# Kernel tuning notes

Measured on AMD Instinct MI355X. Metric: run time of the kernel, lower is better.

## Reference

```python
import jax, jax.numpy as jnp
import numpy as np
import math

N_HEAD = 16
H_DIM = 32            # per-half head dim
LAMBDA_INIT = 0.8 - 0.6 * math.exp(-0.3 * 1)  # depth = 1
EPS = 1e-6


def _rmsnorm(x, scale):
    xf = x.astype(jnp.float32)
    normed = xf * jax.lax.rsqrt(jnp.mean(xf * xf, axis=-1, keepdims=True) + EPS)
    return normed.astype(x.dtype) * scale


def setup_inputs() -> dict:
    key = jax.random.key(0)
    ks = jax.random.split(key, 8)
    B, T, D = 2, 2048, 1024
    return {
        "x": jax.random.normal(ks[0], (B, T, D), jnp.float32),
        "Wqkv": jax.random.normal(ks[1], (D, 3 * D), jnp.float32) * (1.0 / math.sqrt(D)),
        "Wproj": jax.random.normal(ks[2], (D, D), jnp.float32) * (1.0 / math.sqrt(D)),
        "lambda_q1": jax.random.normal(ks[3], (H_DIM,), jnp.float32) * 0.1,
        "lambda_k1": jax.random.normal(ks[4], (H_DIM,), jnp.float32) * 0.1,
        "lambda_q2": jax.random.normal(ks[5], (H_DIM,), jnp.float32) * 0.1,
        "lambda_k2": jax.random.normal(ks[6], (H_DIM,), jnp.float32) * 0.1,
        "rms_scale": jnp.ones((2 * H_DIM,), jnp.float32),
    }


def reference(x, Wqkv, Wproj, lambda_q1, lambda_k1, lambda_q2, lambda_k2, rms_scale):
    B, T, C = x.shape
    H, h = N_HEAD, H_DIM
    qkv = x @ Wqkv                          # [B,T,3C]
    q, k, v = jnp.split(qkv, 3, axis=-1)
    q = q.reshape(B, T, 2 * H, h).transpose(0, 2, 1, 3)   # [B,2H,T,h]
    k = k.reshape(B, T, 2 * H, h).transpose(0, 2, 1, 3)   # [B,2H,T,h]
    v = v.reshape(B, T, H, 2 * h).transpose(0, 2, 1, 3)   # [B,H,T,2h]
    q1, q2 = jnp.split(q, 2, axis=1)        # each [B,H,T,h]
    k1, k2 = jnp.split(k, 2, axis=1)
    scale = 1.0 / math.sqrt(h)

    def sdpa(qh, kh):
        scores = jnp.einsum('bhqd,bhkd->bhqk', qh, kh) * scale
        return jnp.einsum('bhqk,bhkd->bhqd', jax.nn.softmax(scores, axis=-1), v)

    attn1 = sdpa(q1, k1)                    # [B,H,T,2h]
    attn2 = sdpa(q2, k2)
    lam1 = jnp.exp(jnp.sum(lambda_q1 * lambda_k1))
    lam2 = jnp.exp(jnp.sum(lambda_q2 * lambda_k2))
    lam = lam1 - lam2 + LAMBDA_INIT
    out = attn1 - lam * attn2
    out = _rmsnorm(out, rms_scale) * (1.0 - LAMBDA_INIT)
    out = out.transpose(0, 2, 1, 3).reshape(B, T, C)
    return out @ Wproj
```

## Files before the change

kernel.cpp:

```cpp
#include <hip/hip_runtime.h>
#include <cstdint>
#include <cstddef>


typedef short bf16x8 __attribute__((ext_vector_type(8)));
typedef float f32x4  __attribute__((ext_vector_type(4)));
typedef float f32x16 __attribute__((ext_vector_type(16)));
typedef unsigned short u16;
typedef u16 u16x4v __attribute__((ext_vector_type(4)));
typedef unsigned int u32;
typedef u32 u32x2 __attribute__((ext_vector_type(2)));
typedef u32 u32x4 __attribute__((ext_vector_type(4)));

#define LAMBDA_INIT 0.35550906759096926f
#define ONE_MINUS_LAMBDA_INIT 0.6444909324090307f
#define SCORE_SCALE 0.17677669529663687f

__device__ __forceinline__ u16 f2bf(float f) {
  uint32_t u = __float_as_uint(f);
  u += 0x7fffu + ((u >> 16) & 1u);
  return (u16)(u >> 16);
}

__device__ __forceinline__ void gload_lds16(const void* g, void* lds) {
  __builtin_amdgcn_global_load_lds(
      (const __attribute__((address_space(1))) void*)g,
      (__attribute__((address_space(3))) void*)lds, 16, 0, 0);
}

__device__ __forceinline__ u32 cvtpk_bf16(float lo, float hi) {
  u32 r;
  asm("v_cvt_pk_bf16_f32 %0, %1, %2" : "=v"(r) : "v"(lo), "v"(hi));
  return r;
}

__device__ __forceinline__ float xchg32f(float v, int hi) {
  u32x2 r = __builtin_amdgcn_permlane32_swap(__float_as_uint(v), __float_as_uint(v), false, false);
  return __uint_as_float(hi ? r.x : r.y);
}

__device__ __forceinline__ float rmax16(const f32x16& v) {
  float m = v[0];
#pragma unroll
  for (int i = 1; i < 16; ++i) m = fmaxf(m, v[i]);
  return m;
}

__device__ __forceinline__ float rsum16(const f32x16& v) {
  float a = 0.f;
#pragma unroll
  for (int i = 0; i < 16; ++i) a += v[i];
  return a;
}

__global__ void conv_x_kernel(const float* __restrict__ in, u16* __restrict__ out, int n4) {
  int i = blockIdx.x * blockDim.x + threadIdx.x;
  if (i < n4) {
    float4 v = ((const float4*)in)[i];
    u16x4v o;
    o.x = f2bf(v.x); o.y = f2bf(v.y); o.z = f2bf(v.z); o.w = f2bf(v.w);
    ((u16x4v*)out)[i] = o;
  }
}

__global__ void conv_transpose_kernel(const float* __restrict__ W, u16* __restrict__ WT,
                                      int K, int N) {
  __shared__ u16 L[64][72];
  const int n0 = blockIdx.x * 64, k0 = blockIdx.y * 64;
#pragma unroll
  for (int i = 0; i < 16; ++i) {
    int lin = i * 256 + threadIdx.x;
    int rr = lin >> 6, cc = lin & 63;
    L[rr][cc] = f2bf(W[(size_t)(k0 + rr) * N + n0 + cc]);
  }
  __syncthreads();
#pragma unroll
  for (int i = 0; i < 16; ++i) {
    int lin = i * 256 + threadIdx.x;
    int rr = lin >> 6, cc = lin & 63;
    WT[(size_t)(n0 + rr) * K + k0 + cc] = L[cc][rr];
  }
}

template <typename OutT>
__global__ __launch_bounds__(256, 2) void gemm_bt(const u16* __restrict__ A,
                                                  const u16* __restrict__ Bt,
                                                  OutT* __restrict__ C,
                                                  int M, int N, int K) {
  __shared__ __align__(16) u16 As[2][128 * 32];
  __shared__ __align__(16) u16 Bs[2][128 * 32];
  const int wid = threadIdx.x >> 6, lane = threadIdx.x & 63;
  const int l15 = lane & 15, lhi = lane >> 4;
  const int wm = wid >> 1, wn = wid & 1;
  const int tm = blockIdx.x * 128, tn = blockIdx.y * 128;
  const int rr = lane >> 2, cb = (lane & 3) * 8;
  const int nkt = K >> 5;

  f32x4 acc[4][4];
#pragma unroll
  for (int m = 0; m < 4; ++m)
#pragma unroll
    for (int n = 0; n < 4; ++n) acc[m][n] = (f32x4){0.f, 0.f, 0.f, 0.f};

  auto stage = [&](int buf, int kt) {
#pragma unroll
    for (int i = 0; i < 2; ++i) {
      int lr = wid * 32 + i * 16;
      gload_lds16(A + (size_t)(tm + lr + rr) * K + kt * 32 + cb, &As[buf][lr * 32]);
      gload_lds16(Bt + (size_t)(tn + lr + rr) * K + kt * 32 + cb, &Bs[buf][lr * 32]);
    }
  };

  stage(0, 0);
  __syncthreads();
  int buf = 0;
  for (int kt = 0; kt < nkt; ++kt) {
    if (kt + 1 < nkt) stage(buf ^ 1, kt + 1);
    bf16x8 af[4], bfr[4];
#pragma unroll
    for (int m = 0; m < 4; ++m)
      af[m] = *(const bf16x8*)&As[buf][(wm * 64 + m * 16 + l15) * 32 + lhi * 8];
#pragma unroll
    for (int n = 0; n < 4; ++n)
      bfr[n] = *(const bf16x8*)&Bs[buf][(wn * 64 + n * 16 + l15) * 32 + lhi * 8];
#pragma unroll
    for (int m = 0; m < 4; ++m)
#pragma unroll
      for (int n = 0; n < 4; ++n)
        acc[m][n] = __builtin_amdgcn_mfma_f32_16x16x32_bf16(af[m], bfr[n], acc[m][n], 0, 0, 0);
    __syncthreads();
    buf ^= 1;
  }

#pragma unroll
  for (int m = 0; m < 4; ++m)
#pragma unroll
    for (int n = 0; n < 4; ++n)
#pragma unroll
      for (int r = 0; r < 4; ++r) {
        int row = tm + wm * 64 + m * 16 + lhi * 4 + r;
        int col = tn + wn * 64 + n * 16 + l15;
        float v = acc[m][n][r];
        if constexpr (sizeof(OutT) == 2)
          C[(size_t)row * N + col] = (OutT)f2bf(v);
        else
          C[(size_t)row * N + col] = v;
      }
}

#define KLD 32
#define VLD 72

__global__ __launch_bounds__(256, 2) void diff_attn_kernel(
    const u16* __restrict__ qkv,
    const float* __restrict__ lq1, const float* __restrict__ lk1,
    const float* __restrict__ lq2, const float* __restrict__ lk2,
    const float* __restrict__ rms_scale,
    u16* __restrict__ y) {
  __shared__ __align__(16) u16 K1s[2][64 * KLD];
  __shared__ __align__(16) u16 K2s[2][64 * KLD];
  __shared__ __align__(16) u16 VTs[2][64 * VLD];

  const int tid = threadIdx.x;
  const int wid = tid >> 6, lane = tid & 63;
  const int l31 = lane & 31, hi = lane >> 5;

  const int id = blockIdx.x;
  const int swz = (id & 7) * 64 + (id >> 3);
  const int qt = swz & 15;
  const int bh = swz >> 4;
  const int b = bh >> 4, head = bh & 15;
  const size_t row0 = (size_t)b * 2048;

  float d1 = 0.f, d2 = 0.f;
#pragma unroll
  for (int i = 0; i < 32; ++i) { d1 += lq1[i] * lk1[i]; d2 += lq2[i] * lk2[i]; }
  const float lam = expf(d1) - expf(d2) + LAMBDA_INIT;

  const int qrow = qt * 128 + wid * 32 + l31;
  const u16* qrp = qkv + (row0 + qrow) * 3072;
  bf16x8 q1f[2], q2f[2];
#pragma unroll
  for (int c = 0; c < 2; ++c) {
    q1f[c] = *(const bf16x8*)(qrp + head * 32 + c * 16 + hi * 8);
    q2f[c] = *(const bf16x8*)(qrp + 512 + head * 32 + c * 16 + hi * 8);
  }

  f32x16 o1[2], o2[2];
#pragma unroll
  for (int dt = 0; dt < 2; ++dt)
#pragma unroll
    for (int i = 0; i < 16; ++i) { o1[dt][i] = 0.f; o2[dt][i] = 0.f; }
  float m1 = -1e30f, m2 = -1e30f;
  float ls1 = 0.f, ls2 = 0.f;

  auto issueK = [&](int buf, int kt) {
    const size_t krow0 = row0 + (size_t)kt * 64;
    const int srow = wid * 16 + (lane >> 2);
    const int gcol = 8 * ((lane & 3) ^ ((lane >> 3) & 3));
    const u16* g = qkv + (krow0 + srow) * 3072 + 1024 + head * 32 + gcol;
    gload_lds16(g, &K1s[buf][wid * 512]);
    gload_lds16(g + 512, &K2s[buf][wid * 512]);
  };
  auto loadV = [&](int kt, bf16x8* nv) {
    const size_t krow0 = row0 + (size_t)kt * 64;
#pragma unroll
    for (int h2 = 0; h2 < 2; ++h2) {
      int vid = h2 * 256 + tid;
      int vrow = vid >> 3, d0 = (vid & 7) * 8;
      nv[h2] = *(const bf16x8*)(qkv + (krow0 + vrow) * 3072 + 2048 + head * 64 + d0);
    }
  };
  auto writeV = [&](int buf, const bf16x8* nv) {
#pragma unroll
    for (int h2 = 0; h2 < 2; ++h2) {
      int vid = h2 * 256 + tid;
      int vrow = vid >> 3, d0 = (vid & 7) * 8;
      int wrow = vrow ^ (d0 & 56);
#pragma unroll
      for (int e = 0; e < 8; ++e) VTs[buf][(d0 + e) * VLD + wrow] = (u16)nv[h2][e];
    }
  };

  auto process = [&](const bf16x8* qf, const u16* Ks, const bf16x8 (*vf)[2][2],
                     float& m, float& ls, f32x16* o) {
    f32x16 s[2];
#pragma unroll
    for (int t = 0; t < 2; ++t) {
#pragma unroll
      for (int i = 0; i < 16; ++i) s[t][i] = 0.f;
      const int row = t * 32 + l31;
      const int sg = 8 * ((row >> 1) & 3);
#pragma unroll
      for (int c = 0; c < 2; ++c) {
        bf16x8 kf = *(const bf16x8*)&Ks[row * KLD + ((c * 16 + hi * 8) ^ sg)];
        s[t] = __builtin_amdgcn_mfma_f32_32x32x16_bf16(kf, qf[c], s[t], 0, 0, 0);
      }
    }
    float pm = fmaxf(rmax16(s[0]), rmax16(s[1]));
    pm = fmaxf(pm, xchg32f(pm, hi));
    if (!__all(pm - m <= 8.0f)) {
      float mn = fmaxf(m, pm);
      float corr = __expf((m - mn) * SCORE_SCALE);
      m = mn;
      ls *= corr;
#pragma unroll
      for (int dt = 0; dt < 2; ++dt)
#pragma unroll
        for (int i = 0; i < 16; ++i) o[dt][i] *= corr;
    }
#pragma unroll
    for (int t = 0; t < 2; ++t)
#pragma unroll
      for (int i = 0; i < 16; ++i)
        s[t][i] = __expf((s[t][i] - m) * SCORE_SCALE);
    ls += rsum16(s[0]) + rsum16(s[1]);
#pragma unroll
    for (int t = 0; t < 2; ++t) {
      u32 W[4][2];
#pragma unroll
      for (int g = 0; g < 4; ++g)
#pragma unroll
        for (int u = 0; u < 2; ++u)
          W[g][u] = cvtpk_bf16(s[t][4 * g + 2 * u], s[t][4 * g + 2 * u + 1]);
#pragma unroll
      for (int kap = 0; kap < 2; ++kap) {
        u32x2 r0 = __builtin_amdgcn_permlane32_swap(W[2 * kap][0], W[2 * kap + 1][0], false, false);
        u32x2 r1 = __builtin_amdgcn_permlane32_swap(W[2 * kap][1], W[2 * kap + 1][1], false, false);
        u32x4 words = {r0.x, r1.x, r0.y, r1.y};
        bf16x8 pB = __builtin_bit_cast(bf16x8, words);
#pragma unroll
        for (int dt = 0; dt < 2; ++dt)
          o[dt] = __builtin_amdgcn_mfma_f32_32x32x16_bf16(vf[t][kap][dt], pB, o[dt], 0, 0, 0);
      }
    }
  };

  {
    bf16x8 v0[2];
    issueK(0, 0);
    loadV(0, v0);
    writeV(0, v0);
  }
  __syncthreads();

  int buf = 0;
  for (int kt = 0; kt < 32; ++kt) {
    bf16x8 nv[2];
    if (kt + 1 < 32) { issueK(buf ^ 1, kt + 1); loadV(kt + 1, nv); }

    bf16x8 vf[2][2][2];
#pragma unroll
    for (int t = 0; t < 2; ++t)
#pragma unroll
      for (int kap = 0; kap < 2; ++kap)
#pragma unroll
        for (int dt = 0; dt < 2; ++dt) {
          int d = dt * 32 + l31;
          int koff = (t * 32 + kap * 16 + hi * 8) ^ (d & 56);
          vf[t][kap][dt] = *(const bf16x8*)&VTs[buf][d * VLD + koff];
        }

    process(q1f, &K1s[buf][0], vf, m1, ls1, o1);
    process(q2f, &K2s[buf][0], vf, m2, ls2, o2);

    if (kt + 1 < 32) writeV(buf ^ 1, nv);
    __syncthreads();
    buf ^= 1;
  }

  ls1 += xchg32f(ls1, hi);
  ls2 += xchg32f(ls2, hi);
  const float il1 = 1.0f / ls1, il2 = 1.0f / ls2;

  f32x16 v[2];
  float ssq = 0.f;
#pragma unroll
  for (int dt = 0; dt < 2; ++dt)
#pragma unroll
    for (int i = 0; i < 16; ++i) {
      float a = o1[dt][i] * il1 - lam * (o2[dt][i] * il2);
      v[dt][i] = a;
      ssq += a * a;
    }
  ssq += xchg32f(ssq, hi);
  const float inv = rsqrtf(ssq * (1.0f / 64.0f) + 1e-6f);

  u16* yr = y + (row0 + qrow) * 1024 + head * 64;
#pragma unroll
  for (int dt = 0; dt < 2; ++dt)
#pragma unroll
    for (int rg = 0; rg < 4; ++rg) {
      int dbase = 8 * rg + 4 * hi + 32 * dt;
      u16x4v w;
#pragma unroll
      for (int bb = 0; bb < 4; ++bb)
        w[bb] = f2bf(v[dt][4 * rg + bb] * inv * rms_scale[dbase + bb] * ONE_MINUS_LAMBDA_INIT);
      *(u16x4v*)(yr + dbase) = w;
    }
}

extern "C" void kernel_launch(void* const* d_in, const int* in_sizes, int n_in,
                              void* d_out, int out_size, void* d_ws, size_t ws_size,
                              hipStream_t stream) {
  const float* x     = (const float*)d_in[0];
  const float* Wqkv  = (const float*)d_in[1];
  const float* Wproj = (const float*)d_in[2];
  const float* lq1   = (const float*)d_in[3];
  const float* lk1   = (const float*)d_in[4];
  const float* lq2   = (const float*)d_in[5];
  const float* lk2   = (const float*)d_in[6];
  const float* rms   = (const float*)d_in[7];
  float* out = (float*)d_out;

  char* ws = (char*)d_ws;
  u16* xb     = (u16*)(ws);
  u16* WqkvT  = (u16*)(ws + (size_t)(8  << 20));
  u16* WprojT = (u16*)(ws + (size_t)(14 << 20));
  u16* qkvb   = (u16*)(ws + (size_t)(16 << 20));
  u16* yb     = xb;

  conv_x_kernel<<<4096, 256, 0, stream>>>(x, xb, 1048576);
  conv_transpose_kernel<<<dim3(48, 16), 256, 0, stream>>>(Wqkv, WqkvT, 1024, 3072);
  conv_transpose_kernel<<<dim3(16, 16), 256, 0, stream>>>(Wproj, WprojT, 1024, 1024);
  gemm_bt<u16><<<dim3(32, 24), 256, 0, stream>>>(xb, WqkvT, qkvb, 4096, 3072, 1024);
  diff_attn_kernel<<<512, 256, 0, stream>>>(qkvb, lq1, lk1, lq2, lk2, rms, yb);
  gemm_bt<float><<<dim3(32, 8), 256, 0, stream>>>(yb, WprojT, out, 4096, 1024, 1024);
}
```

Measured before the change: 243.5 us.

## Fold softmax scale into Q with exp2, swizzle GEMM tiles, tree reductions

```diff
diff --git a/kernel.cpp b/kernel.cpp
--- a/kernel.cpp
+++ b/kernel.cpp
@@ -15,6 +15,8 @@
 #define LAMBDA_INIT 0.35550906759096926f
 #define ONE_MINUS_LAMBDA_INIT 0.6444909324090307f
 #define SCORE_SCALE 0.17677669529663687f
+#define C2SCALE 0.25503532063484407f
+#define DTHR 2.0402825650787526f
 
 __device__ __forceinline__ u16 f2bf(float f) {
   uint32_t u = __float_as_uint(f);
@@ -40,17 +42,22 @@
 }
 
 __device__ __forceinline__ float rmax16(const f32x16& v) {
-  float m = v[0];
-#pragma unroll
-  for (int i = 1; i < 16; ++i) m = fmaxf(m, v[i]);
-  return m;
+  float a0 = fmaxf(v[0], v[1]),  a1 = fmaxf(v[2], v[3]);
+  float a2 = fmaxf(v[4], v[5]),  a3 = fmaxf(v[6], v[7]);
+  float a4 = fmaxf(v[8], v[9]),  a5 = fmaxf(v[10], v[11]);
+  float a6 = fmaxf(v[12], v[13]), a7 = fmaxf(v[14], v[15]);
+  float b0 = fmaxf(a0, a1), b1 = fmaxf(a2, a3);
+  float b2 = fmaxf(a4, a5), b3 = fmaxf(a6, a7);
+  return fmaxf(fmaxf(b0, b1), fmaxf(b2, b3));
 }
 
 __device__ __forceinline__ float rsum16(const f32x16& v) {
-  float a = 0.f;
-#pragma unroll
-  for (int i = 0; i < 16; ++i) a += v[i];
-  return a;
+  float a0 = v[0] + v[1],  a1 = v[2] + v[3];
+  float a2 = v[4] + v[5],  a3 = v[6] + v[7];
+  float a4 = v[8] + v[9],  a5 = v[10] + v[11];
+  float a6 = v[12] + v[13], a7 = v[14] + v[15];
+  float b0 = a0 + a1, b1 = a2 + a3, b2 = a4 + a5, b3 = a6 + a7;
+  return (b0 + b1) + (b2 + b3);
 }
 
 __global__ void conv_x_kernel(const float* __restrict__ in, u16* __restrict__ out, int n4) {
@@ -92,7 +99,13 @@
   const int wid = threadIdx.x >> 6, lane = threadIdx.x & 63;
   const int l15 = lane & 15, lhi = lane >> 4;
   const int wm = wid >> 1, wn = wid & 1;
-  const int tm = blockIdx.x * 128, tn = blockIdx.y * 128;
+
+  const int gy = N >> 7;
+  const int nwg = (M >> 7) * gy;
+  const int id = blockIdx.x;
+  const int swz = (id & 7) * (nwg >> 3) + (id >> 3);
+  const int tm = (swz / gy) * 128, tn = (swz % gy) * 128;
+
   const int rr = lane >> 2, cb = (lane & 3) * 8;
   const int nkt = K >> 5;
 
@@ -185,6 +198,15 @@
     q1f[c] = *(const bf16x8*)(qrp + head * 32 + c * 16 + hi * 8);
     q2f[c] = *(const bf16x8*)(qrp + 512 + head * 32 + c * 16 + hi * 8);
   }
+#pragma unroll
+  for (int c = 0; c < 2; ++c)
+#pragma unroll
+    for (int e = 0; e < 8; ++e) {
+      float x1 = __uint_as_float(((u32)(u16)q1f[c][e]) << 16) * C2SCALE;
+      float x2 = __uint_as_float(((u32)(u16)q2f[c][e]) << 16) * C2SCALE;
+      q1f[c][e] = (short)f2bf(x1);
+      q2f[c][e] = (short)f2bf(x2);
+    }
 
   f32x16 o1[2], o2[2];
 #pragma unroll
@@ -239,9 +261,9 @@
     }
     float pm = fmaxf(rmax16(s[0]), rmax16(s[1]));
     pm = fmaxf(pm, xchg32f(pm, hi));
-    if (!__all(pm - m <= 8.0f)) {
+    if (!__all(pm - m <= DTHR)) {
       float mn = fmaxf(m, pm);
-      float corr = __expf((m - mn) * SCORE_SCALE);
+      float corr = exp2f(m - mn);
       m = mn;
       ls *= corr;
 #pragma unroll
@@ -253,7 +275,7 @@
     for (int t = 0; t < 2; ++t)
 #pragma unroll
       for (int i = 0; i < 16; ++i)
-        s[t][i] = __expf((s[t][i] - m) * SCORE_SCALE);
+        s[t][i] = exp2f(s[t][i] - m);
     ls += rsum16(s[0]) + rsum16(s[1]);
 #pragma unroll
     for (int t = 0; t < 2; ++t) {
@@ -363,7 +385,7 @@
   conv_x_kernel<<<4096, 256, 0, stream>>>(x, xb, 1048576);
   conv_transpose_kernel<<<dim3(48, 16), 256, 0, stream>>>(Wqkv, WqkvT, 1024, 3072);
   conv_transpose_kernel<<<dim3(16, 16), 256, 0, stream>>>(Wproj, WprojT, 1024, 1024);
-  gemm_bt<u16><<<dim3(32, 24), 256, 0, stream>>>(xb, WqkvT, qkvb, 4096, 3072, 1024);
+  gemm_bt<u16><<<768, 256, 0, stream>>>(xb, WqkvT, qkvb, 4096, 3072, 1024);
   diff_attn_kernel<<<512, 256, 0, stream>>>(qkvb, lq1, lk1, lq2, lk2, rms, yb);
-  gemm_bt<float><<<dim3(32, 8), 256, 0, stream>>>(yb, WprojT, out, 4096, 1024, 1024);
-}
+  gemm_bt<float><<<256, 256, 0, stream>>>(yb, WprojT, out, 4096, 1024, 1024);
+}
```

Result: slower. 261.8 us (+7.5%).
